# Performance work log

Hardware: AMD Instinct MI355X
Metric: run time of the kernel (lower is better)

Reference implementation:

```python
import jax, jax.numpy as jnp
import numpy as np

S, N, MSA_DIM, PAIR_DIM, D, H = 8, 256, 256, 128, 32, 8
EPS = 1e-5


def layer_norm(x, w, b):
    mu = jnp.mean(x, axis=-1, keepdims=True)
    var = jnp.mean((x - mu) ** 2, axis=-1, keepdims=True)
    return (x - mu) * jax.lax.rsqrt(var + EPS) * w + b


def setup_inputs() -> dict:
    key = jax.random.key(0)
    ks = jax.random.split(key, 8)
    def rnd(k, shape, scale=1.0):
        return jax.random.normal(k, shape, jnp.float32) * scale
    return {
        "msa_rep": rnd(ks[0], (S, N, MSA_DIM)),
        "pair_rep": rnd(ks[1], (N, N, PAIR_DIM)),
        "ln_w": jnp.ones((MSA_DIM,), jnp.float32),
        "ln_b": jnp.zeros((MSA_DIM,), jnp.float32),
        "w_qkv": rnd(ks[2], (MSA_DIM, 3 * H * D), 0.02),
        "ln_pair_w": jnp.ones((PAIR_DIM,), jnp.float32),
        "ln_pair_b": jnp.zeros((PAIR_DIM,), jnp.float32),
        "w_b": rnd(ks[3], (PAIR_DIM, H), 0.02),
        "w_g": rnd(ks[4], (MSA_DIM, H * D), 0.02),
        "w_out": rnd(ks[5], (H * D, MSA_DIM), 0.02),
        "b_out": jnp.zeros((MSA_DIM,), jnp.float32),
    }


def reference(msa_rep, pair_rep, ln_w, ln_b, w_qkv, ln_pair_w, ln_pair_b,
              w_b, w_g, w_out, b_out):
    s, n, _ = msa_rep.shape
    x = layer_norm(msa_rep, ln_w, ln_b)                      # [s, n, msa_dim]
    qkv = x @ w_qkv                                          # [s, n, 3*h*d]
    # chunk(3, dim=-1) then view(..., d, h): d outer, h inner
    q, k, v = [t.reshape(s, n, D, H) for t in jnp.split(qkv, 3, axis=-1)]
    # pair bias: LN + linear -> [n, n, h], broadcast to [1, i, j, 1, h]
    b = layer_norm(pair_rep, ln_pair_w, ln_pair_b) @ w_b     # [n, n, h]
    g = jax.nn.sigmoid(x @ w_g).reshape(s, n, D, H)          # gate [s, n, d, h]
    # NOTE: logits keep the d axis (no contraction): einsum 'sidh,sjdh->sijdh'
    scores = (q[:, :, None, :, :] * k[:, None, :, :, :]) * (D ** -0.5) \
             + b[None, :, :, None, :]                        # [s, i, j, d, h]
    a = jax.nn.softmax(scores, axis=2)                       # softmax over j
    out = g * jnp.einsum('sijdh,sjdh->sidh', a, v)           # [s, n, d, h]
    return out.reshape(s, n, D * H) @ w_out + b_out          # [s, n, msa_dim]
```

## Files before the change

kernel.cpp:

```cpp
#include <hip/hip_runtime.h>
#include <math.h>

#define S_DIM 8
#define N_RES 256
#define MSA_DIM 256
#define PAIR_DIM 128
#define D_DIM 32
#define H_DIM 8
#define M_ROWS (S_DIM * N_RES)
#define QKV_N (3 * H_DIM * D_DIM)
#define HD (H_DIM * D_DIM)
#define LOG2E 1.4426950408889634f

#define DPP_ADD(x, ctrl, rmask)                                                \
    x += __int_as_float(__builtin_amdgcn_update_dpp(                           \
        0, __float_as_int(x), (ctrl), (rmask), 0xf, true))

__device__ __forceinline__ float wave_sum63(float x) {
    DPP_ADD(x, 0x111, 0xf);
    DPP_ADD(x, 0x112, 0xf);
    DPP_ADD(x, 0x114, 0xf);
    DPP_ADD(x, 0x118, 0xf);
    DPP_ADD(x, 0x142, 0xa);
    DPP_ADD(x, 0x143, 0xc);
    return x;
}

__device__ __forceinline__ float quad_sum(float x) {
    x += __int_as_float(__builtin_amdgcn_update_dpp(
        0, __float_as_int(x), 0xB1, 0xf, 0xf, true));
    x += __int_as_float(__builtin_amdgcn_update_dpp(
        0, __float_as_int(x), 0x4E, 0xf, 0xf, true));
    return x;
}

__global__ __launch_bounds__(256) void ln_msa_kernel(
    const float* __restrict__ msa, const float* __restrict__ w,
    const float* __restrict__ b, float* __restrict__ x)
{
    int row = blockIdx.x;
    int t = threadIdx.x;
    float v = msa[row * MSA_DIM + t];
    float s1 = wave_sum63(v);
    float s2 = wave_sum63(v * v);
    __shared__ float r1[4], r2[4];
    int wave = t >> 6, lane = t & 63;
    if (lane == 63) { r1[wave] = s1; r2[wave] = s2; }
    __syncthreads();
    float S1 = r1[0] + r1[1] + r1[2] + r1[3];
    float S2 = r2[0] + r2[1] + r2[2] + r2[3];
    float mu = S1 * (1.0f / 256.0f);
    float var = S2 * (1.0f / 256.0f) - mu * mu;
    float rs = rsqrtf(var + 1e-5f);
    x[row * MSA_DIM + t] = (v - mu) * rs * w[t] + b[t];
}

__global__ __launch_bounds__(256) void xw_kernel(
    const float* __restrict__ X, const float* __restrict__ Wqkv,
    const float* __restrict__ Wg, float* __restrict__ q_t,
    float* __restrict__ k_t, float* __restrict__ v_t, float* __restrict__ g_t)
{
    __shared__ float Xs[16][68];
    __shared__ float Ws[16][132];
    int t = threadIdx.x;
    int bx = blockIdx.x;
    int qkv_mode = (bx < 6);
    int n0 = bx * 128;
    const float* W = qkv_mode ? Wqkv : Wg;
    int Ncols = qkv_mode ? QKV_N : HD;
    int wn0 = qkv_mode ? n0 : n0 - QKV_N;
    int m0 = blockIdx.y * 64;
    int tm = t >> 4, tn = t & 15;
    int lxm = t >> 2, lxk = (t & 3) * 4;
    int lwk = t >> 4, lwn = (t & 15) * 8;
    float acc[4][8] = {};
    float4 xa = *(const float4*)&X[(m0 + lxm) * 256 + lxk];
    float4 w0 = *(const float4*)&W[(size_t)lwk * Ncols + wn0 + lwn];
    float4 w1 = *(const float4*)&W[(size_t)lwk * Ncols + wn0 + lwn + 4];
    for (int kt = 0; kt < 16; kt++) {
        __syncthreads();
        Xs[lxk + 0][lxm] = xa.x; Xs[lxk + 1][lxm] = xa.y;
        Xs[lxk + 2][lxm] = xa.z; Xs[lxk + 3][lxm] = xa.w;
        *(float4*)&Ws[lwk][lwn] = w0;
        *(float4*)&Ws[lwk][lwn + 4] = w1;
        __syncthreads();
        if (kt < 15) {
            int kb = (kt + 1) * 16;
            xa = *(const float4*)&X[(m0 + lxm) * 256 + kb + lxk];
            w0 = *(const float4*)&W[(size_t)(kb + lwk) * Ncols + wn0 + lwn];
            w1 = *(const float4*)&W[(size_t)(kb + lwk) * Ncols + wn0 + lwn + 4];
        }
#pragma unroll
        for (int kk = 0; kk < 16; kk++) {
            float a[4], b[8];
            *(float4*)a = *(const float4*)&Xs[kk][tm * 4];
            *(float4*)&b[0] = *(const float4*)&Ws[kk][tn * 4];
            *(float4*)&b[4] = *(const float4*)&Ws[kk][64 + tn * 4];
#pragma unroll
            for (int i = 0; i < 4; i++)
#pragma unroll
                for (int u = 0; u < 8; u++) acc[i][u] += a[i] * b[u];
        }
    }
#pragma unroll
    for (int i = 0; i < 4; i++) {
        int mm = m0 + tm * 4 + i;
#pragma unroll
        for (int u = 0; u < 8; u++) {
            float c = acc[i][u];
            int nn = n0 + (u >> 2) * 64 + tn * 4 + (u & 3);
            if (qkv_mode) {
                int chunk = nn >> 8, r = nn & 255, d = r >> 3, h = r & 7;
                float* dst = (chunk == 0) ? q_t : ((chunk == 1) ? k_t : v_t);
                dst[(h * M_ROWS + mm) * D_DIM + d] = c;
            } else {
                int gn = nn - QKV_N;
                int d = gn >> 3, h = gn & 7;
                g_t[(h * M_ROWS + mm) * D_DIM + d] = 1.0f / (1.0f + __expf(-c));
            }
        }
    }
}

__global__ __launch_bounds__(256) void out_gemm_kernel(
    const float* __restrict__ X, const float* __restrict__ W,
    float* __restrict__ part)
{
    __shared__ float Xs[16][68];
    __shared__ float Ws[16][132];
    int t = threadIdx.x;
    int n0 = blockIdx.x * 128;
    int m0 = blockIdx.y * 64;
    int k0g = blockIdx.z * 64;
    int tm = t >> 4, tn = t & 15;
    int lxm = t >> 2, lxk = (t & 3) * 4;
    int lwk = t >> 4, lwn = (t & 15) * 8;
    float acc[4][8] = {};
    int wr0 = ((k0g + lwk) & 31) * 8 + ((k0g + lwk) >> 5);
    float4 xa = *(const float4*)&X[(m0 + lxm) * 256 + k0g + lxk];
    float4 w0 = *(const float4*)&W[(size_t)wr0 * 256 + n0 + lwn];
    float4 w1 = *(const float4*)&W[(size_t)wr0 * 256 + n0 + lwn + 4];
    for (int kt = 0; kt < 4; kt++) {
        __syncthreads();
        Xs[lxk + 0][lxm] = xa.x; Xs[lxk + 1][lxm] = xa.y;
        Xs[lxk + 2][lxm] = xa.z; Xs[lxk + 3][lxm] = xa.w;
        *(float4*)&Ws[lwk][lwn] = w0;
        *(float4*)&Ws[lwk][lwn + 4] = w1;
        __syncthreads();
        if (kt < 3) {
            int kb = k0g + (kt + 1) * 16;
            int wrow = ((kb + lwk) & 31) * 8 + ((kb + lwk) >> 5);
            xa = *(const float4*)&X[(m0 + lxm) * 256 + kb + lxk];
            w0 = *(const float4*)&W[(size_t)wrow * 256 + n0 + lwn];
            w1 = *(const float4*)&W[(size_t)wrow * 256 + n0 + lwn + 4];
        }
#pragma unroll
        for (int kk = 0; kk < 16; kk++) {
            float a[4], b[8];
            *(float4*)a = *(const float4*)&Xs[kk][tm * 4];
            *(float4*)&b[0] = *(const float4*)&Ws[kk][tn * 4];
            *(float4*)&b[4] = *(const float4*)&Ws[kk][64 + tn * 4];
#pragma unroll
            for (int i = 0; i < 4; i++)
#pragma unroll
                for (int u = 0; u < 8; u++) acc[i][u] += a[i] * b[u];
        }
    }
    float* pb = part + (size_t)blockIdx.z * (M_ROWS * 256);
#pragma unroll
    for (int i = 0; i < 4; i++) {
        int mm = m0 + tm * 4 + i;
        *(float4*)&pb[mm * 256 + n0 + tn * 4] = *(float4*)&acc[i][0];
        *(float4*)&pb[mm * 256 + n0 + 64 + tn * 4] = *(float4*)&acc[i][4];
    }
}

__global__ __launch_bounds__(256) void reduce_out_kernel(
    const float* __restrict__ part, const float* __restrict__ bias,
    float* __restrict__ out)
{
    int idx = blockIdx.x * 256 + threadIdx.x;
    int e = idx * 4;
    int n = e & 255;
    float4 p0 = *(const float4*)&part[e];
    float4 p1 = *(const float4*)&part[e + M_ROWS * 256];
    float4 p2 = *(const float4*)&part[e + 2 * M_ROWS * 256];
    float4 p3 = *(const float4*)&part[e + 3 * M_ROWS * 256];
    float4 bb = *(const float4*)&bias[n];
    float4 o;
    o.x = p0.x + p1.x + p2.x + p3.x + bb.x;
    o.y = p0.y + p1.y + p2.y + p3.y + bb.y;
    o.z = p0.z + p1.z + p2.z + p3.z + bb.z;
    o.w = p0.w + p1.w + p2.w + p3.w + bb.w;
    *(float4*)&out[e] = o;
}

__global__ __launch_bounds__(128) void pb_setup_kernel(
    const float* __restrict__ lw, const float* __restrict__ lb,
    const float* __restrict__ wb, float* __restrict__ Abuf)
{
    __shared__ float P[128][8], Q[128][8];
    int c = threadIdx.x;
    float lwc = lw[c], lbc = lb[c];
#pragma unroll
    for (int h = 0; h < 8; h++) {
        float w = wb[c * 8 + h];
        float a = lwc * w;
        P[c][h] = a;
        Q[c][h] = lbc * w;
        Abuf[c * 12 + h] = a * LOG2E;
    }
    __syncthreads();
    if (c < 8) {
        float s = 0, cc = 0;
        for (int k = 0; k < 128; k++) { s += P[k][c]; cc += Q[k][c]; }
        Abuf[1536 + c] = s * LOG2E;
        Abuf[1544 + c] = cc * LOG2E;
    }
}

__global__ __launch_bounds__(256) void pair_bias_kernel(
    const float* __restrict__ pair, const float* __restrict__ Abuf,
    float* __restrict__ b2)
{
    __shared__ __align__(16) float As[1552];
    int t = threadIdx.x;
    for (int idx = t; idx < 388; idx += 256)
        ((float4*)As)[idx] = ((const float4*)Abuf)[idx];
    __syncthreads();
    int row = blockIdx.x * 64 + (t >> 2);
    int q = t & 3;
    const float* in = pair + (size_t)row * PAIR_DIM;
    float4 x4[8];
#pragma unroll
    for (int it = 0; it < 8; it++)
        x4[it] = *(const float4*)&in[it * 16 + q * 4];
    float s = 0, s2 = 0;
    float dot[8] = {};
#pragma unroll
    for (int it = 0; it < 8; it++) {
        float xk[4];
        *(float4*)xk = x4[it];
#pragma unroll
        for (int k = 0; k < 4; k++) {
            int c = it * 16 + q * 4 + k;
            float xv = xk[k];
            s += xv; s2 += xv * xv;
            float4 A0 = *(const float4*)&As[c * 12];
            float4 A1 = *(const float4*)&As[c * 12 + 4];
            dot[0] += xv * A0.x; dot[1] += xv * A0.y;
            dot[2] += xv * A0.z; dot[3] += xv * A0.w;
            dot[4] += xv * A1.x; dot[5] += xv * A1.y;
            dot[6] += xv * A1.z; dot[7] += xv * A1.w;
        }
    }
    s = quad_sum(s);
    s2 = quad_sum(s2);
#pragma unroll
    for (int h = 0; h < 8; h++) dot[h] = quad_sum(dot[h]);
    float mu = s * (1.0f / 128.0f);
    float var = s2 * (1.0f / 128.0f) - mu * mu;
    float rs = rsqrtf(var + 1e-5f);
    int h0 = q * 2;
#pragma unroll
    for (int u = 0; u < 2; u++) {
        int h = h0 + u;
        b2[h * 65536 + row] = rs * (dot[h] - mu * As[1536 + h]) + As[1544 + h];
    }
}

__global__ __launch_bounds__(256) void attn_kernel(
    const float* __restrict__ q_t, const float* __restrict__ k_t,
    const float* __restrict__ v_t, const float* __restrict__ g_t,
    const float* __restrict__ b2, float* __restrict__ ao)
{
    __shared__ float k_sh[256][32];
    __shared__ float v_sh[256][32];
    int blk = blockIdx.x;
    int s = blk >> 6, h = (blk >> 3) & 7, it = blk & 7;
    int t = threadIdx.x;
    const float* kb = k_t + (size_t)(h * M_ROWS + s * N_RES) * D_DIM;
    const float* vb = v_t + (size_t)(h * M_ROWS + s * N_RES) * D_DIM;
    for (int idx = t; idx < 2048; idx += 256) {
        ((float4*)k_sh)[idx] = ((const float4*)kb)[idx];
        ((float4*)v_sh)[idx] = ((const float4*)vb)[idx];
    }
    __syncthreads();
    int jp = t & 3, dg = (t >> 2) & 7, li = t >> 5;
    int d0 = dg * 4;
    const float SCL2 = 0.17677669529663687f * LOG2E;
    int ig[4], mrow[4];
    float qs[4][4];
#pragma unroll
    for (int r = 0; r < 4; r++) {
        ig[r] = it * 32 + r * 8 + li;
        mrow[r] = s * N_RES + ig[r];
        float4 q4 = *(const float4*)&q_t[(size_t)(h * M_ROWS + mrow[r]) * D_DIM + d0];
        qs[r][0] = q4.x * SCL2; qs[r][1] = q4.y * SCL2;
        qs[r][2] = q4.z * SCL2; qs[r][3] = q4.w * SCL2;
    }
    float den[4][4] = {}, acc[4][4] = {};
    const float* bbase = b2 + h * 65536;
    for (int js4 = 0; js4 < 16; js4++) {
        float bb[4][4];
#pragma unroll
        for (int r = 0; r < 4; r++)
            *(float4*)&bb[r][0] =
                *(const float4*)&bbase[ig[r] * 256 + jp * 64 + js4 * 4];
#pragma unroll
        for (int u = 0; u < 4; u++) {
            int j = jp * 64 + js4 * 4 + u;
            float ka[4], va[4];
            *(float4*)ka = *(const float4*)&k_sh[j][d0];
            *(float4*)va = *(const float4*)&v_sh[j][d0];
#pragma unroll
            for (int r = 0; r < 4; r++) {
#pragma unroll
                for (int c = 0; c < 4; c++) {
                    float e = __builtin_amdgcn_exp2f(qs[r][c] * ka[c] + bb[r][u]);
                    den[r][c] += e;
                    acc[r][c] += e * va[c];
                }
            }
        }
    }
#pragma unroll
    for (int r = 0; r < 4; r++)
#pragma unroll
        for (int c = 0; c < 4; c++) {
            den[r][c] = quad_sum(den[r][c]);
            acc[r][c] = quad_sum(acc[r][c]);
        }
    if (jp == 0) {
#pragma unroll
        for (int r = 0; r < 4; r++) {
            float4 g4 = *(const float4*)&g_t[(size_t)(h * M_ROWS + mrow[r]) * D_DIM + d0];
            float4 o;
            o.x = g4.x * acc[r][0] / den[r][0];
            o.y = g4.y * acc[r][1] / den[r][1];
            o.z = g4.z * acc[r][2] / den[r][2];
            o.w = g4.w * acc[r][3] / den[r][3];
            *(float4*)&ao[(size_t)mrow[r] * HD + h * 32 + d0] = o;
        }
    }
}

extern "C" void kernel_launch(void* const* d_in, const int* in_sizes, int n_in,
                              void* d_out, int out_size, void* d_ws, size_t ws_size,
                              hipStream_t stream)
{
    const float* msa_rep   = (const float*)d_in[0];
    const float* pair_rep  = (const float*)d_in[1];
    const float* ln_w      = (const float*)d_in[2];
    const float* ln_b      = (const float*)d_in[3];
    const float* w_qkv     = (const float*)d_in[4];
    const float* ln_pair_w = (const float*)d_in[5];
    const float* ln_pair_b = (const float*)d_in[6];
    const float* w_b       = (const float*)d_in[7];
    const float* w_g       = (const float*)d_in[8];
    const float* w_out     = (const float*)d_in[9];
    const float* b_out     = (const float*)d_in[10];
    float* out = (float*)d_out;

    float* ws = (float*)d_ws;
    const size_t CH = 524288;
    float* x    = ws + 0 * CH;
    float* q_t  = ws + 1 * CH;
    float* k_t  = ws + 2 * CH;
    float* v_t  = ws + 3 * CH;
    float* g_t  = ws + 4 * CH;
    float* b2   = ws + 5 * CH;
    float* ao   = ws + 6 * CH;
    float* Abuf = ws + 7 * CH;
    float* part = ws + 8 * CH;

    ln_msa_kernel<<<M_ROWS, 256, 0, stream>>>(msa_rep, ln_w, ln_b, x);

    xw_kernel<<<dim3(8, 32), 256, 0, stream>>>(
        x, w_qkv, w_g, q_t, k_t, v_t, g_t);

    pb_setup_kernel<<<1, 128, 0, stream>>>(ln_pair_w, ln_pair_b, w_b, Abuf);

    pair_bias_kernel<<<65536 / 64, 256, 0, stream>>>(pair_rep, Abuf, b2);

    attn_kernel<<<512, 256, 0, stream>>>(q_t, k_t, v_t, g_t, b2, ao);

    out_gemm_kernel<<<dim3(2, 32, 4), 256, 0, stream>>>(ao, w_out, part);

    reduce_out_kernel<<<512, 256, 0, stream>>>(part, b_out, out);
}
```

Measured before the change: 169.2 us.

## Compute QKV/gate projection with split-bf16 MFMA instead of FP32 FMA

Replaces the FP32 scalar-FMA GEMM for the QKV and gate projection with a bf16 MFMA kernel. It uses a hi/lo split (three products: hi*hi, lo*hi, hi*lo) to keep close to FP32 accuracy. LayerNorm now emits bf16 hi/lo pairs, and a new kernel converts and transposes the weights each call. The epilogue stages results through shared memory so q/k/v/g are written as float4 in the head-major layout. This adds an extra launch and some precision risk, in exchange for matrix-core throughput on a GEMM that was compute-bound.

After: 154.7 us. 8.6% less time.

```diff
diff --git a/kernel.cpp b/kernel.cpp
--- a/kernel.cpp
+++ b/kernel.cpp
@@ -10,7 +10,11 @@
 #define M_ROWS (S_DIM * N_RES)
 #define QKV_N (3 * H_DIM * D_DIM)
 #define HD (H_DIM * D_DIM)
+#define XW_N 1024
 #define LOG2E 1.4426950408889634f
+
+typedef __attribute__((ext_vector_type(8))) short short8;
+typedef __attribute__((ext_vector_type(4))) float floatx4;
 
 #define DPP_ADD(x, ctrl, rmask)                                                \
     x += __int_as_float(__builtin_amdgcn_update_dpp(                           \
@@ -34,9 +38,15 @@
     return x;
 }
 
+__device__ __forceinline__ unsigned short bf16rn(float v) {
+    unsigned u = __float_as_uint(v);
+    return (unsigned short)((u + 0x7FFF + ((u >> 16) & 1)) >> 16);
+}
+
 __global__ __launch_bounds__(256) void ln_msa_kernel(
     const float* __restrict__ msa, const float* __restrict__ w,
-    const float* __restrict__ b, float* __restrict__ x)
+    const float* __restrict__ b, unsigned short* __restrict__ xhi,
+    unsigned short* __restrict__ xlo)
 {
     int row = blockIdx.x;
     int t = threadIdx.x;
@@ -52,72 +62,154 @@
     float mu = S1 * (1.0f / 256.0f);
     float var = S2 * (1.0f / 256.0f) - mu * mu;
     float rs = rsqrtf(var + 1e-5f);
-    x[row * MSA_DIM + t] = (v - mu) * rs * w[t] + b[t];
-}
-
-__global__ __launch_bounds__(256) void xw_kernel(
-    const float* __restrict__ X, const float* __restrict__ Wqkv,
-    const float* __restrict__ Wg, float* __restrict__ q_t,
-    float* __restrict__ k_t, float* __restrict__ v_t, float* __restrict__ g_t)
-{
-    __shared__ float Xs[16][68];
-    __shared__ float Ws[16][132];
+    float y = (v - mu) * rs * w[t] + b[t];
+    unsigned short h = bf16rn(y);
+    float hf = __uint_as_float((unsigned)h << 16);
+    unsigned short l = bf16rn(y - hf);
+    xhi[row * 256 + t] = h;
+    xlo[row * 256 + t] = l;
+}
+
+__global__ __launch_bounds__(256) void wconv_kernel(
+    const float* __restrict__ w_qkv, const float* __restrict__ w_g,
+    unsigned short* __restrict__ whiT, unsigned short* __restrict__ wloT)
+{
+    int id = blockIdx.x * 256 + threadIdx.x;
+    int n = id >> 5, oct = id & 31;
+    int k0 = oct * 8;
+    const float* src;
+    int stride;
+    if (n < QKV_N) { src = w_qkv + n; stride = QKV_N; }
+    else           { src = w_g + (n - QKV_N); stride = HD; }
+    unsigned short h8[8], l8[8];
+#pragma unroll
+    for (int j = 0; j < 8; j++) {
+        float v = src[(size_t)(k0 + j) * stride];
+        unsigned short h = bf16rn(v);
+        float hf = __uint_as_float((unsigned)h << 16);
+        h8[j] = h;
+        l8[j] = bf16rn(v - hf);
+    }
+    *(short8*)&whiT[n * 256 + k0] = *(short8*)h8;
+    *(short8*)&wloT[n * 256 + k0] = *(short8*)l8;
+}
+
+__global__ __launch_bounds__(256) void xw_mfma_kernel(
+    const unsigned short* __restrict__ xhi, const unsigned short* __restrict__ xlo,
+    const unsigned short* __restrict__ whiT, const unsigned short* __restrict__ wloT,
+    float* __restrict__ q_t, float* __restrict__ k_t,
+    float* __restrict__ v_t, float* __restrict__ g_t)
+{
+    __shared__ unsigned short As[64 * 72];
+    __shared__ unsigned short Bs[128 * 72];
+    __shared__ float Cs[64 * 132];
     int t = threadIdx.x;
-    int bx = blockIdx.x;
-    int qkv_mode = (bx < 6);
-    int n0 = bx * 128;
-    const float* W = qkv_mode ? Wqkv : Wg;
-    int Ncols = qkv_mode ? QKV_N : HD;
-    int wn0 = qkv_mode ? n0 : n0 - QKV_N;
-    int m0 = blockIdx.y * 64;
-    int tm = t >> 4, tn = t & 15;
-    int lxm = t >> 2, lxk = (t & 3) * 4;
-    int lwk = t >> 4, lwn = (t & 15) * 8;
-    float acc[4][8] = {};
-    float4 xa = *(const float4*)&X[(m0 + lxm) * 256 + lxk];
-    float4 w0 = *(const float4*)&W[(size_t)lwk * Ncols + wn0 + lwn];
-    float4 w1 = *(const float4*)&W[(size_t)lwk * Ncols + wn0 + lwn + 4];
-    for (int kt = 0; kt < 16; kt++) {
+    int n0 = blockIdx.x * 128, m0 = blockIdx.y * 64;
+    int w = t >> 6, L = t & 63;
+    int wm = (w & 1) * 32, wn = (w >> 1) * 64;
+    int l15 = L & 15, l4 = L >> 4;
+
+    int alm = t >> 3, alk = (t & 7) * 8;
+    floatx4 acc[2][4];
+#pragma unroll
+    for (int a = 0; a < 2; a++)
+#pragma unroll
+        for (int b = 0; b < 4; b++) acc[a][b] = (floatx4){0, 0, 0, 0};
+
+    const unsigned short* Asrc = xhi;
+    const unsigned short* Bsrc = whiT;
+    short8 pa0 = *(const short8*)&Asrc[(m0 + alm) * 256 + alk];
+    short8 pa1 = *(const short8*)&Asrc[(m0 + alm + 32) * 256 + alk];
+    short8 pb[4];
+#pragma unroll
+    for (int j = 0; j < 4; j++) {
+        int id = t + 256 * j;
+        int bn = id >> 3, bc = (id & 7) * 8;
+        pb[j] = *(const short8*)&Bsrc[(n0 + bn) * 256 + bc];
+    }
+
+    for (int r = 0; r < 12; r++) {
         __syncthreads();
-        Xs[lxk + 0][lxm] = xa.x; Xs[lxk + 1][lxm] = xa.y;
-        Xs[lxk + 2][lxm] = xa.z; Xs[lxk + 3][lxm] = xa.w;
-        *(float4*)&Ws[lwk][lwn] = w0;
-        *(float4*)&Ws[lwk][lwn + 4] = w1;
+        *(short8*)&As[alm * 72 + alk] = pa0;
+        *(short8*)&As[(alm + 32) * 72 + alk] = pa1;
+#pragma unroll
+        for (int j = 0; j < 4; j++) {
+            int id = t + 256 * j;
+            int bn = id >> 3, bc = (id & 7) * 8;
+            *(short8*)&Bs[bn * 72 + bc] = pb[j];
+        }
         __syncthreads();
-        if (kt < 15) {
-            int kb = (kt + 1) * 16;
-            xa = *(const float4*)&X[(m0 + lxm) * 256 + kb + lxk];
-            w0 = *(const float4*)&W[(size_t)(kb + lwk) * Ncols + wn0 + lwn];
-            w1 = *(const float4*)&W[(size_t)(kb + lwk) * Ncols + wn0 + lwn + 4];
-        }
-#pragma unroll
-        for (int kk = 0; kk < 16; kk++) {
-            float a[4], b[8];
-            *(float4*)a = *(const float4*)&Xs[kk][tm * 4];
-            *(float4*)&b[0] = *(const float4*)&Ws[kk][tn * 4];
-            *(float4*)&b[4] = *(const float4*)&Ws[kk][64 + tn * 4];
-#pragma unroll
-            for (int i = 0; i < 4; i++)
-#pragma unroll
-                for (int u = 0; u < 8; u++) acc[i][u] += a[i] * b[u];
-        }
-    }
-#pragma unroll
-    for (int i = 0; i < 4; i++) {
-        int mm = m0 + tm * 4 + i;
-#pragma unroll
-        for (int u = 0; u < 8; u++) {
-            float c = acc[i][u];
-            int nn = n0 + (u >> 2) * 64 + tn * 4 + (u & 3);
-            if (qkv_mode) {
-                int chunk = nn >> 8, r = nn & 255, d = r >> 3, h = r & 7;
-                float* dst = (chunk == 0) ? q_t : ((chunk == 1) ? k_t : v_t);
-                dst[(h * M_ROWS + mm) * D_DIM + d] = c;
-            } else {
-                int gn = nn - QKV_N;
-                int d = gn >> 3, h = gn & 7;
-                g_t[(h * M_ROWS + mm) * D_DIM + d] = 1.0f / (1.0f + __expf(-c));
+        if (r < 11) {
+            int rn = r + 1;
+            int seg = rn >> 2, kb = (rn & 3) * 64;
+            const unsigned short* An = (seg == 1) ? xlo : xhi;
+            const unsigned short* Bn = (seg == 2) ? wloT : whiT;
+            pa0 = *(const short8*)&An[(m0 + alm) * 256 + kb + alk];
+            pa1 = *(const short8*)&An[(m0 + alm + 32) * 256 + kb + alk];
+#pragma unroll
+            for (int j = 0; j < 4; j++) {
+                int id = t + 256 * j;
+                int bn = id >> 3, bc = (id & 7) * 8;
+                pb[j] = *(const short8*)&Bn[(n0 + bn) * 256 + kb + bc];
             }
+        }
+#pragma unroll
+        for (int ks = 0; ks < 2; ks++) {
+            int ko = ks * 32 + l4 * 8;
+            short8 af[2], bf[4];
+#pragma unroll
+            for (int a = 0; a < 2; a++)
+                af[a] = *(short8*)&As[(wm + a * 16 + l15) * 72 + ko];
+#pragma unroll
+            for (int b = 0; b < 4; b++)
+                bf[b] = *(short8*)&Bs[(wn + b * 16 + l15) * 72 + ko];
+#pragma unroll
+            for (int a = 0; a < 2; a++)
+#pragma unroll
+                for (int b = 0; b < 4; b++)
+                    acc[a][b] = __builtin_amdgcn_mfma_f32_16x16x32_bf16(
+                        af[a], bf[b], acc[a][b], 0, 0, 0);
+        }
+    }
+
+#pragma unroll
+    for (int a = 0; a < 2; a++)
+#pragma unroll
+        for (int b = 0; b < 4; b++) {
+            int nl = wn + b * 16 + l15;
+#pragma unroll
+            for (int rg = 0; rg < 4; rg++) {
+                int ml = wm + a * 16 + l4 * 4 + rg;
+                Cs[ml * 132 + nl] = acc[a][b][rg];
+            }
+        }
+    __syncthreads();
+    int qkv_mode = (n0 < QKV_N);
+    int chunk = n0 >> 8;
+    int dbase = (n0 & 255) >> 3;
+#pragma unroll
+    for (int j = 0; j < 8; j++) {
+        int id = t + 256 * j;
+        int m = id >> 5;
+        int h = (id >> 2) & 7;
+        int dq = id & 3;
+        float vals[4];
+#pragma unroll
+        for (int jj = 0; jj < 4; jj++)
+            vals[jj] = Cs[m * 132 + (dq * 4 + jj) * 8 + h];
+        int mm = m0 + m;
+        int daddr = dbase + dq * 4;
+        if (qkv_mode) {
+            float* dst = (chunk == 0) ? q_t : ((chunk == 1) ? k_t : v_t);
+            *(float4*)&dst[(size_t)(h * M_ROWS + mm) * D_DIM + daddr] =
+                *(float4*)vals;
+        } else {
+            float4 o;
+            o.x = 1.0f / (1.0f + __expf(-vals[0]));
+            o.y = 1.0f / (1.0f + __expf(-vals[1]));
+            o.z = 1.0f / (1.0f + __expf(-vals[2]));
+            o.w = 1.0f / (1.0f + __expf(-vals[3]));
+            *(float4*)&g_t[(size_t)(h * M_ROWS + mm) * D_DIM + daddr] = o;
         }
     }
 }
@@ -364,20 +456,25 @@
 
     float* ws = (float*)d_ws;
     const size_t CH = 524288;
-    float* x    = ws + 0 * CH;
-    float* q_t  = ws + 1 * CH;
-    float* k_t  = ws + 2 * CH;
-    float* v_t  = ws + 3 * CH;
-    float* g_t  = ws + 4 * CH;
-    float* b2   = ws + 5 * CH;
-    float* ao   = ws + 6 * CH;
-    float* Abuf = ws + 7 * CH;
-    float* part = ws + 8 * CH;
-
-    ln_msa_kernel<<<M_ROWS, 256, 0, stream>>>(msa_rep, ln_w, ln_b, x);
-
-    xw_kernel<<<dim3(8, 32), 256, 0, stream>>>(
-        x, w_qkv, w_g, q_t, k_t, v_t, g_t);
+    float* q_t  = ws + 0 * CH;
+    float* k_t  = ws + 1 * CH;
+    float* v_t  = ws + 2 * CH;
+    float* g_t  = ws + 3 * CH;
+    float* b2   = ws + 4 * CH;
+    float* ao   = ws + 5 * CH;
+    float* Abuf = ws + 6 * CH;
+    float* part = ws + 7 * CH;
+    unsigned short* xhi  = (unsigned short*)(ws + 11 * CH);
+    unsigned short* xlo  = xhi + M_ROWS * 256;
+    unsigned short* whiT = (unsigned short*)(ws + 12 * CH);
+    unsigned short* wloT = whiT + XW_N * 256;
+
+    wconv_kernel<<<128, 256, 0, stream>>>(w_qkv, w_g, whiT, wloT);
+
+    ln_msa_kernel<<<M_ROWS, 256, 0, stream>>>(msa_rep, ln_w, ln_b, xhi, xlo);
+
+    xw_mfma_kernel<<<dim3(8, 32), 256, 0, stream>>>(
+        xhi, xlo, whiT, wloT, q_t, k_t, v_t, g_t);
 
     pb_setup_kernel<<<1, 128, 0, stream>>>(ln_pair_w, ln_pair_b, w_b, Abuf);
 
```
